# Kernel optimization log

Measured on AMD Instinct MI355X. Metric: run time of the kernel, lower is better.

The kernel has to match this reference:

```python
import jax, jax.numpy as jnp
from jax import lax
import numpy as np

POOL = 9   # nms_threshold*2 + 1
PAD = 4    # POOL // 2


def setup_inputs() -> dict:
    key = jax.random.key(0)
    x = jax.random.normal(key, (4, 256, 200, 320), dtype=jnp.float32)
    return {"x": x}


def reference(x):
    # x: [B, C, H, W]
    depth_wise_max = jnp.max(x, axis=1, keepdims=True)          # [B,1,H,W]
    is_depth_wise_max = x == depth_wise_max                      # [B,C,H,W] bool
    # 9x9 local max pool, stride 1, pad 4 (torch pads with -inf for max_pool2d)
    local_max = lax.reduce_window(
        x, -jnp.inf, lax.max,
        window_dimensions=(1, 1, POOL, POOL),
        window_strides=(1, 1, 1, 1),
        padding=[(0, 0), (0, 0), (PAD, PAD), (PAD, PAD)],
    )
    is_local_max = x == local_max
    prob = jnp.where(is_depth_wise_max & is_local_max, x, jnp.zeros((), x.dtype)).sum(axis=1)  # [B,H,W]
    return prob
```

## Files before the change

kernel.cpp:

```cpp
#include <hip/hip_runtime.h>
#include <math.h>

#define B_   4
#define C_   256
#define H_   200
#define W_   320
#define HW   (H_ * W_)
#define BHW  (B_ * HW)

#define TH   50
#define TW   64
#define PR   58
#define HSTR 68
#define XSTR 68
#define CS   16
#define CPG  (C_ / CS)
#define NT   512

#define HBUF (PR * HSTR)
#define XBUF (TH * XSTR)

static_assert(TH * 4 == H_, "H tiling");
static_assert(TW * 5 == W_, "W tiling");

__device__ __forceinline__ float max3f(float a, float b, float c) {
  return fmaxf(fmaxf(a, b), c);
}

__device__ __forceinline__ void win9m3(const float v[16], float w[8]) {
  float m3[14];
#pragma unroll
  for (int i = 0; i < 14; ++i) m3[i] = max3f(v[i], v[i + 1], v[i + 2]);
#pragma unroll
  for (int i = 0; i < 8; ++i)  w[i] = max3f(m3[i], m3[i + 3], m3[i + 6]);
}

#define LD4(p, o) (*reinterpret_cast<const float4*>((p) + (o)))

__global__ __launch_bounds__(NT, 4) void hdm_main(const float* __restrict__ x,
                                                  float* __restrict__ wsM,
                                                  float* __restrict__ wsP) {
  __shared__ float hmax[2 * HBUF];
  __shared__ float xcen[2 * XBUF];

  const int tile = blockIdx.x;
  const int b    = blockIdx.y;
  const int cg   = blockIdx.z;
  const int th = tile / 5, tw = tile % 5;
  const int h0 = th * TH, w0 = tw * TW;
  const int tid = (int)threadIdx.x;

  const float* xg = x + (size_t)(b * C_ + cg * CPG) * HW;

  const bool act1 = tid < PR * 8;
  const int  r1   = tid >> 3, s1 = tid & 7;
  const int  gh   = h0 - 4 + r1;
  const bool rok  = (gh >= 0) && (gh < H_);
  const int  gw   = w0 - 4 + s1 * 8;
  const bool lft  = (gw < 0), rgt = (gw + 16 > W_);
  const int  gwc  = lft ? 0 : (rgt ? (W_ - 16) : gw);
  const int  ghc  = min(max(gh, 0), H_ - 1);
  const float* p1 = xg + (size_t)ghc * W_ + gwc;
  const bool wx   = (r1 >= 4) && (r1 <= 53);

  const bool act2 = tid < 448;
  const int  rs2  = tid >> 6, cw2 = tid & 63, r02 = rs2 * 8;
  const int  kv   = (rs2 == 6) ? 2 : 8;

  float accM[8], accP[8];
#pragma unroll
  for (int i = 0; i < 8; ++i) { accM[i] = -INFINITY; accP[i] = 0.f; }

  float4 A0, A1, A2, A3;
  if (act1) {
    A0 = LD4(p1, 0); A1 = LD4(p1, 4); A2 = LD4(p1, 8); A3 = LD4(p1, 12);
    p1 += HW;
  }

  for (int cc = 0; cc < CPG; ++cc) {
    float wH[8];
    float4 xlo, xhi;
    {
      const float tt[16] = {A0.x, A0.y, A0.z, A0.w, A1.x, A1.y, A1.z, A1.w,
                            A2.x, A2.y, A2.z, A2.w, A3.x, A3.y, A3.z, A3.w};
      float v[16];
#pragma unroll
      for (int j = 0; j < 16; ++j) {
        const float va = (j >= 4)  ? tt[j - 4] : -INFINITY;
        const float vb = (j < 12)  ? tt[j + 4] : -INFINITY;
        v[j] = lft ? va : (rgt ? vb : tt[j]);
      }
      win9m3(v, wH);
#pragma unroll
      for (int i = 0; i < 8; ++i) wH[i] = rok ? wH[i] : -INFINITY;
      xlo = make_float4(v[4], v[5], v[6], v[7]);
      xhi = make_float4(v[8], v[9], v[10], v[11]);
    }

    if (act1 && (cc + 1 < CPG)) {
      A0 = LD4(p1, 0); A1 = LD4(p1, 4); A2 = LD4(p1, 8); A3 = LD4(p1, 12);
      p1 += HW;
    }

    float* hb = &hmax[(cc & 1) * HBUF];
    float* xb = &xcen[(cc & 1) * XBUF];
    if (act1) {
      float* hr = hb + r1 * HSTR + s1 * 8;
      *reinterpret_cast<float4*>(hr + 0) = make_float4(wH[0], wH[1], wH[2], wH[3]);
      *reinterpret_cast<float4*>(hr + 4) = make_float4(wH[4], wH[5], wH[6], wH[7]);
      if (wx) {
        float* xr = xb + (r1 - 4) * XSTR + s1 * 8;
        *reinterpret_cast<float4*>(xr + 0) = xlo;
        *reinterpret_cast<float4*>(xr + 4) = xhi;
      }
    }

    __syncthreads();

    if (act2) {
      float hv[16];
#pragma unroll
      for (int i = 0; i < 16; ++i) {
        const int r = min(r02 + i, PR - 1);
        hv[i] = hb[r * HSTR + cw2];
      }
      float w9[8];
      win9m3(hv, w9);
#pragma unroll
      for (int i = 0; i < 8; ++i) {
        if (i < kv) {
          const float xc  = xb[(r02 + i) * XSTR + cw2];
          const float add = (xc == w9[i]) ? xc : 0.f;
          const bool  gt  = xc > accM[i];
          const bool  eq  = xc == accM[i];
          accP[i] = gt ? add : (accP[i] + (eq ? add : 0.f));
          accM[i] = gt ? xc : accM[i];
        }
      }
    }
  }

  if (act2) {
    const size_t obase = (size_t)cg * BHW + (size_t)b * HW;
#pragma unroll
    for (int i = 0; i < 8; ++i) {
      if (i < kv) {
        const size_t idx = obase + (size_t)(h0 + r02 + i) * W_ + (w0 + cw2);
        wsM[idx] = accM[i];
        wsP[idx] = accP[i];
      }
    }
  }
}

__global__ __launch_bounds__(256) void hdm_combine(const float* __restrict__ wsM,
                                                   const float* __restrict__ wsP,
                                                   float* __restrict__ out) {
  const int px = blockIdx.x * 256 + (int)threadIdx.x;
  if (px >= BHW) return;
  float gm = -INFINITY, p = 0.f;
#pragma unroll
  for (int cs = 0; cs < CS; ++cs) {
    const float m = wsM[(size_t)cs * BHW + px];
    const float q = wsP[(size_t)cs * BHW + px];
    const bool gt = m > gm;
    const bool eq = m == gm;
    p  = gt ? q : (p + (eq ? q : 0.f));
    gm = gt ? m : gm;
  }
  out[px] = p;
}

extern "C" void kernel_launch(void* const* d_in, const int* in_sizes, int n_in,
                              void* d_out, int out_size, void* d_ws, size_t ws_size,
                              hipStream_t stream) {
  const float* x = (const float*)d_in[0];
  float* wsM = (float*)d_ws;
  float* wsP = wsM + (size_t)CS * BHW;
  float* out = (float*)d_out;

  hipLaunchKernelGGL(hdm_main, dim3(20, B_, CS), dim3(NT), 0, stream, x, wsM, wsP);
  hipLaunchKernelGGL(hdm_combine, dim3((BHW + 255) / 256), dim3(256), 0, stream,
                     wsM, wsP, out);
}
```

Baseline: 368.4 us.

## Drop LDS center buffer, reload centers from global, specialize edge handling

Result: slower. 567.6 us (+54.1%).

```diff
diff --git a/kernel.cpp b/kernel.cpp
--- a/kernel.cpp
+++ b/kernel.cpp
@@ -12,13 +12,10 @@
 #define TW   64
 #define PR   58
 #define HSTR 68
-#define XSTR 68
 #define CS   16
 #define CPG  (C_ / CS)
 #define NT   512
-
 #define HBUF (PR * HSTR)
-#define XBUF (TH * XSTR)
 
 static_assert(TH * 4 == H_, "H tiling");
 static_assert(TW * 5 == W_, "W tiling");
@@ -27,21 +24,12 @@
   return fmaxf(fmaxf(a, b), c);
 }
 
-__device__ __forceinline__ void win9m3(const float v[16], float w[8]) {
-  float m3[14];
-#pragma unroll
-  for (int i = 0; i < 14; ++i) m3[i] = max3f(v[i], v[i + 1], v[i + 2]);
-#pragma unroll
-  for (int i = 0; i < 8; ++i)  w[i] = max3f(m3[i], m3[i + 3], m3[i + 6]);
-}
-
 #define LD4(p, o) (*reinterpret_cast<const float4*>((p) + (o)))
 
-__global__ __launch_bounds__(NT, 4) void hdm_main(const float* __restrict__ x,
+__global__ __launch_bounds__(NT, 8) void hdm_main(const float* __restrict__ x,
                                                   float* __restrict__ wsM,
                                                   float* __restrict__ wsP) {
   __shared__ float hmax[2 * HBUF];
-  __shared__ float xcen[2 * XBUF];
 
   const int tile = blockIdx.x;
   const int b    = blockIdx.y;
@@ -61,81 +49,100 @@
   const int  gwc  = lft ? 0 : (rgt ? (W_ - 16) : gw);
   const int  ghc  = min(max(gh, 0), H_ - 1);
   const float* p1 = xg + (size_t)ghc * W_ + gwc;
-  const bool wx   = (r1 >= 4) && (r1 <= 53);
 
-  const bool act2 = tid < 448;
-  const int  rs2  = tid >> 6, cw2 = tid & 63, r02 = rs2 * 8;
+  const bool edgeW = (tw == 0) || (tw == 4);
+  const bool edgeH = (th == 0) || (th == 3);
+
+  const int  rs2  = tid >> 6, cw2 = tid & 63;
+  const bool act2 = rs2 < 7;
+  const int  r02  = rs2 * 8;
   const int  kv   = (rs2 == 6) ? 2 : 8;
+  const float* p2 = xg + (size_t)h0 * W_ + (w0 + cw2);
 
   float accM[8], accP[8];
 #pragma unroll
   for (int i = 0; i < 8; ++i) { accM[i] = -INFINITY; accP[i] = 0.f; }
 
   float4 A0, A1, A2, A3;
-  if (act1) {
-    A0 = LD4(p1, 0); A1 = LD4(p1, 4); A2 = LD4(p1, 8); A3 = LD4(p1, 12);
-    p1 += HW;
-  }
+  if (act1) { A0 = LD4(p1, 0); A1 = LD4(p1, 4); A2 = LD4(p1, 8); A3 = LD4(p1, 12); }
 
   for (int cc = 0; cc < CPG; ++cc) {
-    float wH[8];
-    float4 xlo, xhi;
+    float wF[8];
     {
-      const float tt[16] = {A0.x, A0.y, A0.z, A0.w, A1.x, A1.y, A1.z, A1.w,
-                            A2.x, A2.y, A2.z, A2.w, A3.x, A3.y, A3.z, A3.w};
-      float v[16];
+      const float t[16] = {A0.x, A0.y, A0.z, A0.w, A1.x, A1.y, A1.z, A1.w,
+                           A2.x, A2.y, A2.z, A2.w, A3.x, A3.y, A3.z, A3.w};
+      float m3[14];
 #pragma unroll
-      for (int j = 0; j < 16; ++j) {
-        const float va = (j >= 4)  ? tt[j - 4] : -INFINITY;
-        const float vb = (j < 12)  ? tt[j + 4] : -INFINITY;
-        v[j] = lft ? va : (rgt ? vb : tt[j]);
+      for (int i = 0; i < 14; ++i) m3[i] = max3f(t[i], t[i + 1], t[i + 2]);
+      float w[8];
+#pragma unroll
+      for (int i = 0; i < 8; ++i) w[i] = max3f(m3[i], m3[i + 3], m3[i + 6]);
+#pragma unroll
+      for (int i = 0; i < 8; ++i) wF[i] = w[i];
+      if (edgeW) {
+        const float d0 = max3f(m3[0], m3[2], t[4]);
+        const float d1 = fmaxf(d0, t[5]);
+        const float d2 = fmaxf(d1, t[6]);
+        const float d3 = fmaxf(d2, t[7]);
+        const float s8  = max3f(m3[8],  m3[11], m3[13]);
+        const float s9  = max3f(m3[9],  m3[12], t[15]);
+        const float s10 = fmaxf(m3[10], m3[13]);
+        const float s11 = fmaxf(m3[11], m3[13]);
+        wF[0] = lft ? d0 : (rgt ? w[4] : w[0]);
+        wF[1] = lft ? d1 : (rgt ? w[5] : w[1]);
+        wF[2] = lft ? d2 : (rgt ? w[6] : w[2]);
+        wF[3] = lft ? d3 : (rgt ? w[7] : w[3]);
+        wF[4] = lft ? w[0] : (rgt ? s8  : w[4]);
+        wF[5] = lft ? w[1] : (rgt ? s9  : w[5]);
+        wF[6] = lft ? w[2] : (rgt ? s10 : w[6]);
+        wF[7] = lft ? w[3] : (rgt ? s11 : w[7]);
       }
-      win9m3(v, wH);
+      if (edgeH) {
 #pragma unroll
-      for (int i = 0; i < 8; ++i) wH[i] = rok ? wH[i] : -INFINITY;
-      xlo = make_float4(v[4], v[5], v[6], v[7]);
-      xhi = make_float4(v[8], v[9], v[10], v[11]);
-    }
-
-    if (act1 && (cc + 1 < CPG)) {
-      A0 = LD4(p1, 0); A1 = LD4(p1, 4); A2 = LD4(p1, 8); A3 = LD4(p1, 12);
-      p1 += HW;
+        for (int i = 0; i < 8; ++i) wF[i] = rok ? wF[i] : -INFINITY;
+      }
     }
 
     float* hb = &hmax[(cc & 1) * HBUF];
-    float* xb = &xcen[(cc & 1) * XBUF];
     if (act1) {
       float* hr = hb + r1 * HSTR + s1 * 8;
-      *reinterpret_cast<float4*>(hr + 0) = make_float4(wH[0], wH[1], wH[2], wH[3]);
-      *reinterpret_cast<float4*>(hr + 4) = make_float4(wH[4], wH[5], wH[6], wH[7]);
-      if (wx) {
-        float* xr = xb + (r1 - 4) * XSTR + s1 * 8;
-        *reinterpret_cast<float4*>(xr + 0) = xlo;
-        *reinterpret_cast<float4*>(xr + 4) = xhi;
-      }
+      *reinterpret_cast<float4*>(hr + 0) = make_float4(wF[0], wF[1], wF[2], wF[3]);
+      *reinterpret_cast<float4*>(hr + 4) = make_float4(wF[4], wF[5], wF[6], wF[7]);
     }
 
     __syncthreads();
 
+    if (act1 && (cc + 1 < CPG)) {
+      p1 += HW;
+      A0 = LD4(p1, 0); A1 = LD4(p1, 4); A2 = LD4(p1, 8); A3 = LD4(p1, 12);
+    }
+
     if (act2) {
+      const float* pc = p2 + (size_t)cc * HW;
+      float xc[8];
+#pragma unroll
+      for (int i = 0; i < 8; ++i) {
+        const int ri = min(r02 + i, TH - 1);
+        xc[i] = pc[(size_t)ri * W_];
+      }
       float hv[16];
 #pragma unroll
       for (int i = 0; i < 16; ++i) {
         const int r = min(r02 + i, PR - 1);
         hv[i] = hb[r * HSTR + cw2];
       }
-      float w9[8];
-      win9m3(hv, w9);
+      float m3v[14];
+#pragma unroll
+      for (int i = 0; i < 14; ++i) m3v[i] = max3f(hv[i], hv[i + 1], hv[i + 2]);
 #pragma unroll
       for (int i = 0; i < 8; ++i) {
-        if (i < kv) {
-          const float xc  = xb[(r02 + i) * XSTR + cw2];
-          const float add = (xc == w9[i]) ? xc : 0.f;
-          const bool  gt  = xc > accM[i];
-          const bool  eq  = xc == accM[i];
-          accP[i] = gt ? add : (accP[i] + (eq ? add : 0.f));
-          accM[i] = gt ? xc : accM[i];
-        }
+        const float w9  = max3f(m3v[i], m3v[i + 3], m3v[i + 6]);
+        const float xc_ = xc[i];
+        const float add = (xc_ == w9) ? xc_ : 0.f;
+        const bool  gt  = xc_ > accM[i];
+        const bool  eq  = xc_ == accM[i];
+        accP[i] = gt ? add : (accP[i] + (eq ? add : 0.f));
+        accM[i] = gt ? xc_ : accM[i];
       }
     }
   }
```
